# Optimization experiments

Hardware: AMD Instinct MI355X
Metric: run time of the kernel (lower is better)

The kernel has to match this reference:

```python
import jax, jax.numpy as jnp
import numpy as np

D_MODEL = 1024
HEAD_SIZE = 64

def setup_inputs() -> dict:
    key = jax.random.key(0)
    ks = jax.random.split(key, 7)
    s = 1.0 / np.sqrt(D_MODEL)
    return {
        "x": jax.random.normal(ks[0], (4, 2048, D_MODEL), dtype=jnp.float32),
        "wq": jax.random.uniform(ks[1], (D_MODEL, HEAD_SIZE), jnp.float32, -s, s),
        "bq": jax.random.uniform(ks[2], (HEAD_SIZE,), jnp.float32, -s, s),
        "wk": jax.random.uniform(ks[3], (D_MODEL, HEAD_SIZE), jnp.float32, -s, s),
        "bk": jax.random.uniform(ks[4], (HEAD_SIZE,), jnp.float32, -s, s),
        "wv": jax.random.uniform(ks[5], (D_MODEL, HEAD_SIZE), jnp.float32, -s, s),
        "bv": jax.random.uniform(ks[6], (HEAD_SIZE,), jnp.float32, -s, s),
    }

def reference(x, wq, bq, wk, bk, wv, bv):
    # x: [b, n, d_model]; projections -> [b, n, head_size]
    q = x @ wq + bq
    k = x @ wk + bk
    v = x @ wv + bv
    scores = jnp.einsum("bnd,bmd->bnm", q, k) / jnp.sqrt(jnp.float32(HEAD_SIZE))
    attn = jax.nn.softmax(scores, axis=-1)  # [b, n, n]
    return jnp.einsum("bnm,bmd->bnd", attn, v)
```

## Files before the change

kernel.cpp:

```cpp
#include <hip/hip_runtime.h>
#include <math.h>

#define D_MODEL 1024
#define HEAD 64
#define SEQ 2048
#define BATCH 4

typedef _Float16 f16x4 __attribute__((ext_vector_type(4)));
typedef _Float16 f16x8 __attribute__((ext_vector_type(8)));
typedef float f32x4 __attribute__((ext_vector_type(4)));

__global__ __launch_bounds__(256) void prep_w(
    const float* __restrict__ wq, const float* __restrict__ wk,
    const float* __restrict__ wv, _Float16* __restrict__ wT)
{
    const float* w = (blockIdx.y == 0) ? wq : (blockIdx.y == 1) ? wk : wv;
    const int kbase = blockIdx.x * 64;
    __shared__ float t[64][65];
    const int tid = threadIdx.x;
    #pragma unroll
    for (int i = 0; i < 16; i++) {
        int idx = tid + i * 256;
        int kk = idx >> 6, c = idx & 63;
        t[kk][c] = w[(size_t)(kbase + kk) * 64 + c];
    }
    __syncthreads();
    #pragma unroll
    for (int i = 0; i < 16; i++) {
        int idx = tid + i * 256;
        int c = idx >> 6, kk = idx & 63;
        wT[(size_t)(blockIdx.y * 64 + c) * 1024 + kbase + kk] = (_Float16)t[kk][c];
    }
}

__global__ __launch_bounds__(768, 6) void proj_kernel(
    const float* __restrict__ x, const _Float16* __restrict__ wT,
    const float* __restrict__ bq, const float* __restrict__ bk2,
    const float* __restrict__ bv,
    _Float16* __restrict__ q, _Float16* __restrict__ k, _Float16* __restrict__ vT)
{
    const int tid = threadIdx.x;
    const int wave = tid >> 6;
    const int lane = tid & 63;
    const int l16 = lane & 15;
    const int quad = lane >> 4;
    const int row0 = blockIdx.x * 16;

    __shared__ __align__(16) _Float16 Xs[2][16][136];

    const int srow = tid >> 5;
    const int sc4 = tid & 31;
    const float4* xg = reinterpret_cast<const float4*>(x)
                     + (size_t)(row0 + srow) * (D_MODEL / 4) + sc4;

    const _Float16* wp = wT + (size_t)(wave * 16 + l16) * D_MODEL + quad * 8;

    float4 xr;
    if (tid < 512) {
        xr = xg[0];
        f16x4 h;
        h[0] = (_Float16)xr.x; h[1] = (_Float16)xr.y;
        h[2] = (_Float16)xr.z; h[3] = (_Float16)xr.w;
        *(f16x4*)&Xs[0][srow][sc4 * 4] = h;
    }

    f32x4 acc = (f32x4){0.f, 0.f, 0.f, 0.f};

    #pragma unroll 1
    for (int c = 0; c < 8; c++) {
        __syncthreads();
        f16x8 bw0 = *(const f16x8*)(wp + c * 128);
        f16x8 bw1 = *(const f16x8*)(wp + c * 128 + 32);
        f16x8 bw2 = *(const f16x8*)(wp + c * 128 + 64);
        f16x8 bw3 = *(const f16x8*)(wp + c * 128 + 96);
        if (c < 7 && tid < 512) xr = xg[(c + 1) * 32];
        const int bsel = c & 1;
        f16x8 aX0 = *(const f16x8*)&Xs[bsel][l16][0 * 32 + quad * 8];
        f16x8 aX1 = *(const f16x8*)&Xs[bsel][l16][1 * 32 + quad * 8];
        f16x8 aX2 = *(const f16x8*)&Xs[bsel][l16][2 * 32 + quad * 8];
        f16x8 aX3 = *(const f16x8*)&Xs[bsel][l16][3 * 32 + quad * 8];
        acc = __builtin_amdgcn_mfma_f32_16x16x32_f16(aX0, bw0, acc, 0, 0, 0);
        acc = __builtin_amdgcn_mfma_f32_16x16x32_f16(aX1, bw1, acc, 0, 0, 0);
        acc = __builtin_amdgcn_mfma_f32_16x16x32_f16(aX2, bw2, acc, 0, 0, 0);
        acc = __builtin_amdgcn_mfma_f32_16x16x32_f16(aX3, bw3, acc, 0, 0, 0);
        if (c < 7 && tid < 512) {
            f16x4 h;
            h[0] = (_Float16)xr.x; h[1] = (_Float16)xr.y;
            h[2] = (_Float16)xr.z; h[3] = (_Float16)xr.w;
            *(f16x4*)&Xs[bsel ^ 1][srow][sc4 * 4] = h;
        }
    }

    const int g = wave * 16 + l16;
    const int batch = row0 / SEQ;
    const int rbase = row0 + quad * 4;
    if (g < 64) {
        float bias = bq[g];
        #pragma unroll
        for (int r = 0; r < 4; r++)
            q[(size_t)(rbase + r) * HEAD + g] = (_Float16)((acc[r] + bias) * 0.125f);
    } else if (g < 128) {
        float bias = bk2[g - 64];
        #pragma unroll
        for (int r = 0; r < 4; r++)
            k[(size_t)(rbase + r) * HEAD + (g - 64)] = (_Float16)(acc[r] + bias);
    } else {
        float bias = bv[g - 128];
        f16x4 pk;
        #pragma unroll
        for (int r = 0; r < 4; r++) pk[r] = (_Float16)(acc[r] + bias);
        const int seq0 = row0 - batch * SEQ + quad * 4;
        *(f16x4*)(vT + (size_t)(batch * HEAD + (g - 128)) * SEQ + seq0) = pk;
    }
}

__global__ __launch_bounds__(512, 4) void attn_kernel(
    const _Float16* __restrict__ q, const _Float16* __restrict__ k,
    const _Float16* __restrict__ vT, float* __restrict__ out)
{
    const int tid = threadIdx.x;
    const int wave = tid >> 6;
    const int lane = tid & 63;
    const int l16 = lane & 15;
    const int quad = lane >> 4;
    const int b = blockIdx.y;
    const int q0 = blockIdx.x * 16;

    __shared__ __align__(16) char SM[2 * 18432 + 2 * 17408];
    _Float16 (*Ks)[128][72] = (_Float16(*)[128][72])SM;
    _Float16 (*Vs)[64][136] = (_Float16(*)[64][136])(SM + 2 * 18432);
    float (*Oall)[16][68] = (float(*)[16][68])SM;
    __shared__ float Lall[8][16];

    f16x8 bQ[2];
    {
        const _Float16* qp = q + (size_t)(b * SEQ + q0 + l16) * HEAD + quad * 8;
        bQ[0] = *(const f16x8*)qp;
        bQ[1] = *(const f16x8*)(qp + 32);
    }

    f32x4 O[4];
    #pragma unroll
    for (int dt = 0; dt < 4; dt++) O[dt] = (f32x4){0.f, 0.f, 0.f, 0.f};
    float lpart = 0.f;

    const _Float16* kb = k + (size_t)b * SEQ * HEAD;
    const _Float16* vb = vT + (size_t)b * HEAD * SEQ;

    const int krow = tid >> 3, kc8 = (tid & 7) * 8;
    const int vrow = tid >> 4, vc8 = (tid & 15) * 8;
    const _Float16* kg = kb + (size_t)krow * HEAD + kc8;
    const _Float16* vg = vb + (size_t)vrow * SEQ + vc8;

    f16x8 kr0 = *(const f16x8*)kg;
    f16x8 kr1 = *(const f16x8*)(kg + (size_t)64 * HEAD);
    f16x8 vr0 = *(const f16x8*)vg;
    f16x8 vr1 = *(const f16x8*)(vg + (size_t)32 * SEQ);
    *(f16x8*)&Ks[0][krow][kc8] = kr0;
    *(f16x8*)&Ks[0][krow + 64][kc8] = kr1;
    *(f16x8*)&Vs[0][vrow][vc8] = vr0;
    *(f16x8*)&Vs[0][vrow + 32][vc8] = vr1;

    #pragma unroll 1
    for (int c = 0; c < 16; c++) {
        __syncthreads();
        if (c < 15) {
            const int kc2 = (c + 1) * 128;
            kr0 = *(const f16x8*)(kg + (size_t)kc2 * HEAD);
            kr1 = *(const f16x8*)(kg + (size_t)(kc2 + 64) * HEAD);
            vr0 = *(const f16x8*)(vg + kc2);
            vr1 = *(const f16x8*)(vg + (size_t)32 * SEQ + kc2);
        }
        const int bsel = c & 1;
        f16x8 aK0 = *(const f16x8*)&Ks[bsel][wave * 16 + l16][quad * 8];
        f16x8 aK1 = *(const f16x8*)&Ks[bsel][wave * 16 + l16][32 + quad * 8];
        f32x4 st = __builtin_amdgcn_mfma_f32_16x16x32_f16(aK0, bQ[0], (f32x4){0.f, 0.f, 0.f, 0.f}, 0, 0, 0);
        st = __builtin_amdgcn_mfma_f32_16x16x32_f16(aK1, bQ[1], st, 0, 0, 0);

        float p0 = __expf(st[0]);
        float p1 = __expf(st[1]);
        float p2 = __expf(st[2]);
        float p3 = __expf(st[3]);
        lpart += (p0 + p1) + (p2 + p3);
        f16x4 bP;
        bP[0] = (_Float16)p0; bP[1] = (_Float16)p1;
        bP[2] = (_Float16)p2; bP[3] = (_Float16)p3;

        #pragma unroll
        for (int dt = 0; dt < 4; dt++) {
            f16x4 aV = *(const f16x4*)&Vs[bsel][dt * 16 + l16][wave * 16 + quad * 4];
            O[dt] = __builtin_amdgcn_mfma_f32_16x16x16f16(aV, bP, O[dt], 0, 0, 0);
        }
        if (c < 15) {
            *(f16x8*)&Ks[bsel ^ 1][krow][kc8] = kr0;
            *(f16x8*)&Ks[bsel ^ 1][krow + 64][kc8] = kr1;
            *(f16x8*)&Vs[bsel ^ 1][vrow][vc8] = vr0;
            *(f16x8*)&Vs[bsel ^ 1][vrow + 32][vc8] = vr1;
        }
    }
    __syncthreads();

    lpart += __shfl_xor(lpart, 16);
    lpart += __shfl_xor(lpart, 32);
    if (lane < 16) Lall[wave][l16] = lpart;
    #pragma unroll
    for (int dt = 0; dt < 4; dt++)
        #pragma unroll
        for (int r = 0; r < 4; r++)
            Oall[wave][l16][dt * 16 + quad * 4 + r] = O[dt][r];
    __syncthreads();

    {
        int qi = tid >> 5;
        int dd = (tid & 31) * 2;
        float L = 0.f, o0 = 0.f, o1 = 0.f;
        #pragma unroll
        for (int w = 0; w < 8; w++) {
            L += Lall[w][qi];
            o0 += Oall[w][qi][dd];
            o1 += Oall[w][qi][dd + 1];
        }
        float inv = 1.f / L;
        float2 res = make_float2(o0 * inv, o1 * inv);
        *(float2*)(out + (size_t)(b * SEQ + q0 + qi) * HEAD + dd) = res;
    }
}

extern "C" void kernel_launch(void* const* d_in, const int* in_sizes, int n_in,
                              void* d_out, int out_size, void* d_ws, size_t ws_size,
                              hipStream_t stream) {
    const float* x  = (const float*)d_in[0];
    const float* wq = (const float*)d_in[1];
    const float* bq = (const float*)d_in[2];
    const float* wk = (const float*)d_in[3];
    const float* bk = (const float*)d_in[4];
    const float* wv = (const float*)d_in[5];
    const float* bv = (const float*)d_in[6];
    float* out = (float*)d_out;

    const size_t proj_elems = (size_t)BATCH * SEQ * HEAD;
    _Float16* qh = (_Float16*)d_ws;
    _Float16* kh = qh + proj_elems;
    _Float16* vT = kh + proj_elems;
    _Float16* wT = vT + proj_elems;

    prep_w<<<dim3(16, 3), 256, 0, stream>>>(wq, wk, wv, wT);
    proj_kernel<<<dim3(BATCH * SEQ / 16), 768, 0, stream>>>(x, wT, bq, bk, bv, qh, kh, vT);
    attn_kernel<<<dim3(SEQ / 16, BATCH), 512, 0, stream>>>(qh, kh, vT, out);
}
```

Measured before the change: 124.0 us.

## Load K/V fragments directly into registers, process 32 queries per block

The attention kernel no longer stages K and V tiles in shared memory. Each wave loads its own K and transposed-V MFMA fragments straight from global memory into registers, with next-chunk prefetch and no per-iteration barriers. Each block now handles two 16-query tiles so every fragment load feeds twice as much MFMA work, at the cost of more registers and half as many blocks. The projection kernel is fully unrolled and prefetches x four chunks ahead to hide global-load latency.

```diff
diff --git a/kernel.cpp b/kernel.cpp
--- a/kernel.cpp
+++ b/kernel.cpp
@@ -55,25 +55,37 @@
 
     const _Float16* wp = wT + (size_t)(wave * 16 + l16) * D_MODEL + quad * 8;
 
-    float4 xr;
+    float4 xr[4];
     if (tid < 512) {
-        xr = xg[0];
+        xr[0] = xg[0];
+        xr[1] = xg[32];
+        xr[2] = xg[64];
+        xr[3] = xg[96];
         f16x4 h;
-        h[0] = (_Float16)xr.x; h[1] = (_Float16)xr.y;
-        h[2] = (_Float16)xr.z; h[3] = (_Float16)xr.w;
+        h[0] = (_Float16)xr[0].x; h[1] = (_Float16)xr[0].y;
+        h[2] = (_Float16)xr[0].z; h[3] = (_Float16)xr[0].w;
         *(f16x4*)&Xs[0][srow][sc4 * 4] = h;
     }
 
     f32x4 acc = (f32x4){0.f, 0.f, 0.f, 0.f};
 
-    #pragma unroll 1
+    #pragma unroll
     for (int c = 0; c < 8; c++) {
         __syncthreads();
         f16x8 bw0 = *(const f16x8*)(wp + c * 128);
         f16x8 bw1 = *(const f16x8*)(wp + c * 128 + 32);
         f16x8 bw2 = *(const f16x8*)(wp + c * 128 + 64);
         f16x8 bw3 = *(const f16x8*)(wp + c * 128 + 96);
-        if (c < 7 && tid < 512) xr = xg[(c + 1) * 32];
+        if (tid < 512) {
+            if (c + 4 < 8) xr[c & 3] = xg[(c + 4) * 32];
+            if (c < 7) {
+                float4 f = xr[(c + 1) & 3];
+                f16x4 h;
+                h[0] = (_Float16)f.x; h[1] = (_Float16)f.y;
+                h[2] = (_Float16)f.z; h[3] = (_Float16)f.w;
+                *(f16x4*)&Xs[(c + 1) & 1][srow][sc4 * 4] = h;
+            }
+        }
         const int bsel = c & 1;
         f16x8 aX0 = *(const f16x8*)&Xs[bsel][l16][0 * 32 + quad * 8];
         f16x8 aX1 = *(const f16x8*)&Xs[bsel][l16][1 * 32 + quad * 8];
@@ -83,12 +95,6 @@
         acc = __builtin_amdgcn_mfma_f32_16x16x32_f16(aX1, bw1, acc, 0, 0, 0);
         acc = __builtin_amdgcn_mfma_f32_16x16x32_f16(aX2, bw2, acc, 0, 0, 0);
         acc = __builtin_amdgcn_mfma_f32_16x16x32_f16(aX3, bw3, acc, 0, 0, 0);
-        if (c < 7 && tid < 512) {
-            f16x4 h;
-            h[0] = (_Float16)xr.x; h[1] = (_Float16)xr.y;
-            h[2] = (_Float16)xr.z; h[3] = (_Float16)xr.w;
-            *(f16x4*)&Xs[bsel ^ 1][srow][sc4 * 4] = h;
-        }
     }
 
     const int g = wave * 16 + l16;
@@ -124,105 +130,112 @@
     const int l16 = lane & 15;
     const int quad = lane >> 4;
     const int b = blockIdx.y;
-    const int q0 = blockIdx.x * 16;
-
-    __shared__ __align__(16) char SM[2 * 18432 + 2 * 17408];
-    _Float16 (*Ks)[128][72] = (_Float16(*)[128][72])SM;
-    _Float16 (*Vs)[64][136] = (_Float16(*)[64][136])(SM + 2 * 18432);
-    float (*Oall)[16][68] = (float(*)[16][68])SM;
-    __shared__ float Lall[8][16];
-
-    f16x8 bQ[2];
-    {
-        const _Float16* qp = q + (size_t)(b * SEQ + q0 + l16) * HEAD + quad * 8;
-        bQ[0] = *(const f16x8*)qp;
-        bQ[1] = *(const f16x8*)(qp + 32);
-    }
-
-    f32x4 O[4];
-    #pragma unroll
-    for (int dt = 0; dt < 4; dt++) O[dt] = (f32x4){0.f, 0.f, 0.f, 0.f};
-    float lpart = 0.f;
-
-    const _Float16* kb = k + (size_t)b * SEQ * HEAD;
-    const _Float16* vb = vT + (size_t)b * HEAD * SEQ;
-
-    const int krow = tid >> 3, kc8 = (tid & 7) * 8;
-    const int vrow = tid >> 4, vc8 = (tid & 15) * 8;
-    const _Float16* kg = kb + (size_t)krow * HEAD + kc8;
-    const _Float16* vg = vb + (size_t)vrow * SEQ + vc8;
-
-    f16x8 kr0 = *(const f16x8*)kg;
-    f16x8 kr1 = *(const f16x8*)(kg + (size_t)64 * HEAD);
-    f16x8 vr0 = *(const f16x8*)vg;
-    f16x8 vr1 = *(const f16x8*)(vg + (size_t)32 * SEQ);
-    *(f16x8*)&Ks[0][krow][kc8] = kr0;
-    *(f16x8*)&Ks[0][krow + 64][kc8] = kr1;
-    *(f16x8*)&Vs[0][vrow][vc8] = vr0;
-    *(f16x8*)&Vs[0][vrow + 32][vc8] = vr1;
+    const int q0 = blockIdx.x * 32;
+
+    __shared__ float Oall[8][32][68];
+    __shared__ float Lall[8][32];
+
+    f16x8 bQ[2][2];
+    #pragma unroll
+    for (int qt = 0; qt < 2; qt++) {
+        const _Float16* qp = q + (size_t)(b * SEQ + q0 + qt * 16 + l16) * HEAD + quad * 8;
+        bQ[qt][0] = *(const f16x8*)qp;
+        bQ[qt][1] = *(const f16x8*)(qp + 32);
+    }
+
+    f32x4 O[2][4];
+    #pragma unroll
+    for (int qt = 0; qt < 2; qt++)
+        #pragma unroll
+        for (int dt = 0; dt < 4; dt++) O[qt][dt] = (f32x4){0.f, 0.f, 0.f, 0.f};
+    float lp0 = 0.f, lp1 = 0.f;
+
+    const _Float16* kg = k + (size_t)b * SEQ * HEAD
+                       + (size_t)(wave * 16 + l16) * HEAD + quad * 8;
+    const _Float16* vg = vT + (size_t)b * HEAD * SEQ
+                       + (size_t)l16 * SEQ + wave * 16 + quad * 4;
+
+    f16x8 ck0 = *(const f16x8*)kg;
+    f16x8 ck1 = *(const f16x8*)(kg + 32);
+    f16x4 cv0 = *(const f16x4*)(vg);
+    f16x4 cv1 = *(const f16x4*)(vg + 16 * SEQ);
+    f16x4 cv2 = *(const f16x4*)(vg + 32 * SEQ);
+    f16x4 cv3 = *(const f16x4*)(vg + 48 * SEQ);
 
     #pragma unroll 1
     for (int c = 0; c < 16; c++) {
-        __syncthreads();
+        f16x8 nk0, nk1;
+        f16x4 nv0, nv1, nv2, nv3;
         if (c < 15) {
-            const int kc2 = (c + 1) * 128;
-            kr0 = *(const f16x8*)(kg + (size_t)kc2 * HEAD);
-            kr1 = *(const f16x8*)(kg + (size_t)(kc2 + 64) * HEAD);
-            vr0 = *(const f16x8*)(vg + kc2);
-            vr1 = *(const f16x8*)(vg + (size_t)32 * SEQ + kc2);
-        }
-        const int bsel = c & 1;
-        f16x8 aK0 = *(const f16x8*)&Ks[bsel][wave * 16 + l16][quad * 8];
-        f16x8 aK1 = *(const f16x8*)&Ks[bsel][wave * 16 + l16][32 + quad * 8];
-        f32x4 st = __builtin_amdgcn_mfma_f32_16x16x32_f16(aK0, bQ[0], (f32x4){0.f, 0.f, 0.f, 0.f}, 0, 0, 0);
-        st = __builtin_amdgcn_mfma_f32_16x16x32_f16(aK1, bQ[1], st, 0, 0, 0);
-
-        float p0 = __expf(st[0]);
-        float p1 = __expf(st[1]);
-        float p2 = __expf(st[2]);
-        float p3 = __expf(st[3]);
-        lpart += (p0 + p1) + (p2 + p3);
-        f16x4 bP;
-        bP[0] = (_Float16)p0; bP[1] = (_Float16)p1;
-        bP[2] = (_Float16)p2; bP[3] = (_Float16)p3;
-
-        #pragma unroll
-        for (int dt = 0; dt < 4; dt++) {
-            f16x4 aV = *(const f16x4*)&Vs[bsel][dt * 16 + l16][wave * 16 + quad * 4];
-            O[dt] = __builtin_amdgcn_mfma_f32_16x16x16f16(aV, bP, O[dt], 0, 0, 0);
+            const _Float16* kp = kg + (size_t)(c + 1) * 128 * HEAD;
+            nk0 = *(const f16x8*)kp;
+            nk1 = *(const f16x8*)(kp + 32);
+            const _Float16* vp = vg + (c + 1) * 128;
+            nv0 = *(const f16x4*)(vp);
+            nv1 = *(const f16x4*)(vp + 16 * SEQ);
+            nv2 = *(const f16x4*)(vp + 32 * SEQ);
+            nv3 = *(const f16x4*)(vp + 48 * SEQ);
+        }
+        f16x4 bP[2];
+        #pragma unroll
+        for (int qt = 0; qt < 2; qt++) {
+            f32x4 st = __builtin_amdgcn_mfma_f32_16x16x32_f16(ck0, bQ[qt][0], (f32x4){0.f, 0.f, 0.f, 0.f}, 0, 0, 0);
+            st = __builtin_amdgcn_mfma_f32_16x16x32_f16(ck1, bQ[qt][1], st, 0, 0, 0);
+            float p0 = __expf(st[0]);
+            float p1 = __expf(st[1]);
+            float p2 = __expf(st[2]);
+            float p3 = __expf(st[3]);
+            if (qt == 0) lp0 += (p0 + p1) + (p2 + p3);
+            else         lp1 += (p0 + p1) + (p2 + p3);
+            f16x4 bp;
+            bp[0] = (_Float16)p0; bp[1] = (_Float16)p1;
+            bp[2] = (_Float16)p2; bp[3] = (_Float16)p3;
+            bP[qt] = bp;
+        }
+        #pragma unroll
+        for (int qt = 0; qt < 2; qt++) {
+            O[qt][0] = __builtin_amdgcn_mfma_f32_16x16x16f16(cv0, bP[qt], O[qt][0], 0, 0, 0);
+            O[qt][1] = __builtin_amdgcn_mfma_f32_16x16x16f16(cv1, bP[qt], O[qt][1], 0, 0, 0);
+            O[qt][2] = __builtin_amdgcn_mfma_f32_16x16x16f16(cv2, bP[qt], O[qt][2], 0, 0, 0);
+            O[qt][3] = __builtin_amdgcn_mfma_f32_16x16x16f16(cv3, bP[qt], O[qt][3], 0, 0, 0);
         }
         if (c < 15) {
-            *(f16x8*)&Ks[bsel ^ 1][krow][kc8] = kr0;
-            *(f16x8*)&Ks[bsel ^ 1][krow + 64][kc8] = kr1;
-            *(f16x8*)&Vs[bsel ^ 1][vrow][vc8] = vr0;
-            *(f16x8*)&Vs[bsel ^ 1][vrow + 32][vc8] = vr1;
-        }
-    }
+            ck0 = nk0; ck1 = nk1;
+            cv0 = nv0; cv1 = nv1; cv2 = nv2; cv3 = nv3;
+        }
+    }
+
+    lp0 += __shfl_xor(lp0, 16); lp0 += __shfl_xor(lp0, 32);
+    lp1 += __shfl_xor(lp1, 16); lp1 += __shfl_xor(lp1, 32);
+    if (lane < 16) {
+        Lall[wave][l16] = lp0;
+        Lall[wave][16 + l16] = lp1;
+    }
+    #pragma unroll
+    for (int qt = 0; qt < 2; qt++)
+        #pragma unroll
+        for (int dt = 0; dt < 4; dt++)
+            #pragma unroll
+            for (int r = 0; r < 4; r++)
+                Oall[wave][qt * 16 + l16][dt * 16 + quad * 4 + r] = O[qt][dt][r];
     __syncthreads();
 
-    lpart += __shfl_xor(lpart, 16);
-    lpart += __shfl_xor(lpart, 32);
-    if (lane < 16) Lall[wave][l16] = lpart;
-    #pragma unroll
-    for (int dt = 0; dt < 4; dt++)
-        #pragma unroll
-        for (int r = 0; r < 4; r++)
-            Oall[wave][l16][dt * 16 + quad * 4 + r] = O[dt][r];
-    __syncthreads();
-
     {
-        int qi = tid >> 5;
-        int dd = (tid & 31) * 2;
-        float L = 0.f, o0 = 0.f, o1 = 0.f;
+        int qi = tid >> 4;
+        int dg = tid & 15;
+        float L = 0.f;
+        float o[4] = {0.f, 0.f, 0.f, 0.f};
         #pragma unroll
         for (int w = 0; w < 8; w++) {
             L += Lall[w][qi];
-            o0 += Oall[w][qi][dd];
-            o1 += Oall[w][qi][dd + 1];
+            #pragma unroll
+            for (int j = 0; j < 4; j++) o[j] += Oall[w][qi][dg * 4 + j];
         }
         float inv = 1.f / L;
-        float2 res = make_float2(o0 * inv, o1 * inv);
-        *(float2*)(out + (size_t)(b * SEQ + q0 + qi) * HEAD + dd) = res;
+        float4 res;
+        res.x = o[0] * inv; res.y = o[1] * inv;
+        res.z = o[2] * inv; res.w = o[3] * inv;
+        *(float4*)(out + (size_t)(b * SEQ + q0 + qi) * HEAD + dg * 4) = res;
     }
 }
 
@@ -246,5 +259,5 @@
 
     prep_w<<<dim3(16, 3), 256, 0, stream>>>(wq, wk, wv, wT);
     proj_kernel<<<dim3(BATCH * SEQ / 16), 768, 0, stream>>>(x, wT, bq, bk, bv, qh, kh, vT);
-    attn_kernel<<<dim3(SEQ / 16, BATCH), 512, 0, stream>>>(qh, kh, vT, out);
-}
+    attn_kernel<<<dim3(SEQ / 32, BATCH), 512, 0, stream>>>(qh, kh, vT, out);
+}
```

Measured after the change: 131.0 us. 5.7% more time.

## Split projection kernel into dedicated producer wave loading x and MFMA consumer waves

Applied to the files above, without the earlier changes.

Adds a 13th wave (896 threads) to the projection kernel that only loads fp32 x rows, converts them to fp16 and writes the double-buffered LDS tile. The 12 compute waves now only load weights and issue MFMAs. Previously the first 8 compute waves also carried the x loads. The intent is warp specialization, so global x loads overlap with MFMA work. The cost is a larger block and a lower occupancy target (7 waves per SIMD-limited bound). The producer still waits at the same per-chunk barrier, so load latency is only hidden by one stage of prefetch.

```diff
diff --git a/kernel.cpp b/kernel.cpp
--- a/kernel.cpp
+++ b/kernel.cpp
@@ -33,7 +33,7 @@
     }
 }
 
-__global__ __launch_bounds__(768, 6) void proj_kernel(
+__global__ __launch_bounds__(896, 7) void proj_kernel(
     const float* __restrict__ x, const _Float16* __restrict__ wT,
     const float* __restrict__ bq, const float* __restrict__ bk2,
     const float* __restrict__ bv,
@@ -48,20 +48,31 @@
 
     __shared__ __align__(16) _Float16 Xs[2][16][136];
 
-    const int srow = tid >> 5;
-    const int sc4 = tid & 31;
-    const float4* xg = reinterpret_cast<const float4*>(x)
-                     + (size_t)(row0 + srow) * (D_MODEL / 4) + sc4;
+    const bool producer = (wave >= 12);
+
+    const int tid2 = tid - 768;
+    const int srow = (tid2 >> 3) & 15;
+    const int kg = (tid2 & 7) * 16;
+    const float* xp = x + (size_t)(row0 + srow) * D_MODEL + kg;
 
     const _Float16* wp = wT + (size_t)(wave * 16 + l16) * D_MODEL + quad * 8;
 
-    float4 xr;
-    if (tid < 512) {
-        xr = xg[0];
-        f16x4 h;
-        h[0] = (_Float16)xr.x; h[1] = (_Float16)xr.y;
-        h[2] = (_Float16)xr.z; h[3] = (_Float16)xr.w;
-        *(f16x4*)&Xs[0][srow][sc4 * 4] = h;
+    if (producer) {
+        float4 f0 = *(const float4*)(xp);
+        float4 f1 = *(const float4*)(xp + 4);
+        float4 f2 = *(const float4*)(xp + 8);
+        float4 f3 = *(const float4*)(xp + 12);
+        f16x8 h0, h1;
+        h0[0] = (_Float16)f0.x; h0[1] = (_Float16)f0.y;
+        h0[2] = (_Float16)f0.z; h0[3] = (_Float16)f0.w;
+        h0[4] = (_Float16)f1.x; h0[5] = (_Float16)f1.y;
+        h0[6] = (_Float16)f1.z; h0[7] = (_Float16)f1.w;
+        h1[0] = (_Float16)f2.x; h1[1] = (_Float16)f2.y;
+        h1[2] = (_Float16)f2.z; h1[3] = (_Float16)f2.w;
+        h1[4] = (_Float16)f3.x; h1[5] = (_Float16)f3.y;
+        h1[6] = (_Float16)f3.z; h1[7] = (_Float16)f3.w;
+        *(f16x8*)&Xs[0][srow][kg] = h0;
+        *(f16x8*)&Xs[0][srow][kg + 8] = h1;
     }
 
     f32x4 acc = (f32x4){0.f, 0.f, 0.f, 0.f};
@@ -69,48 +80,63 @@
     #pragma unroll 1
     for (int c = 0; c < 8; c++) {
         __syncthreads();
-        f16x8 bw0 = *(const f16x8*)(wp + c * 128);
-        f16x8 bw1 = *(const f16x8*)(wp + c * 128 + 32);
-        f16x8 bw2 = *(const f16x8*)(wp + c * 128 + 64);
-        f16x8 bw3 = *(const f16x8*)(wp + c * 128 + 96);
-        if (c < 7 && tid < 512) xr = xg[(c + 1) * 32];
-        const int bsel = c & 1;
-        f16x8 aX0 = *(const f16x8*)&Xs[bsel][l16][0 * 32 + quad * 8];
-        f16x8 aX1 = *(const f16x8*)&Xs[bsel][l16][1 * 32 + quad * 8];
-        f16x8 aX2 = *(const f16x8*)&Xs[bsel][l16][2 * 32 + quad * 8];
-        f16x8 aX3 = *(const f16x8*)&Xs[bsel][l16][3 * 32 + quad * 8];
-        acc = __builtin_amdgcn_mfma_f32_16x16x32_f16(aX0, bw0, acc, 0, 0, 0);
-        acc = __builtin_amdgcn_mfma_f32_16x16x32_f16(aX1, bw1, acc, 0, 0, 0);
-        acc = __builtin_amdgcn_mfma_f32_16x16x32_f16(aX2, bw2, acc, 0, 0, 0);
-        acc = __builtin_amdgcn_mfma_f32_16x16x32_f16(aX3, bw3, acc, 0, 0, 0);
-        if (c < 7 && tid < 512) {
-            f16x4 h;
-            h[0] = (_Float16)xr.x; h[1] = (_Float16)xr.y;
-            h[2] = (_Float16)xr.z; h[3] = (_Float16)xr.w;
-            *(f16x4*)&Xs[bsel ^ 1][srow][sc4 * 4] = h;
-        }
-    }
-
-    const int g = wave * 16 + l16;
-    const int batch = row0 / SEQ;
-    const int rbase = row0 + quad * 4;
-    if (g < 64) {
-        float bias = bq[g];
-        #pragma unroll
-        for (int r = 0; r < 4; r++)
-            q[(size_t)(rbase + r) * HEAD + g] = (_Float16)((acc[r] + bias) * 0.125f);
-    } else if (g < 128) {
-        float bias = bk2[g - 64];
-        #pragma unroll
-        for (int r = 0; r < 4; r++)
-            k[(size_t)(rbase + r) * HEAD + (g - 64)] = (_Float16)(acc[r] + bias);
-    } else {
-        float bias = bv[g - 128];
-        f16x4 pk;
-        #pragma unroll
-        for (int r = 0; r < 4; r++) pk[r] = (_Float16)(acc[r] + bias);
-        const int seq0 = row0 - batch * SEQ + quad * 4;
-        *(f16x4*)(vT + (size_t)(batch * HEAD + (g - 128)) * SEQ + seq0) = pk;
+        if (!producer) {
+            f16x8 bw0 = *(const f16x8*)(wp + c * 128);
+            f16x8 bw1 = *(const f16x8*)(wp + c * 128 + 32);
+            f16x8 bw2 = *(const f16x8*)(wp + c * 128 + 64);
+            f16x8 bw3 = *(const f16x8*)(wp + c * 128 + 96);
+            const int bsel = c & 1;
+            f16x8 aX0 = *(const f16x8*)&Xs[bsel][l16][0 * 32 + quad * 8];
+            f16x8 aX1 = *(const f16x8*)&Xs[bsel][l16][1 * 32 + quad * 8];
+            f16x8 aX2 = *(const f16x8*)&Xs[bsel][l16][2 * 32 + quad * 8];
+            f16x8 aX3 = *(const f16x8*)&Xs[bsel][l16][3 * 32 + quad * 8];
+            acc = __builtin_amdgcn_mfma_f32_16x16x32_f16(aX0, bw0, acc, 0, 0, 0);
+            acc = __builtin_amdgcn_mfma_f32_16x16x32_f16(aX1, bw1, acc, 0, 0, 0);
+            acc = __builtin_amdgcn_mfma_f32_16x16x32_f16(aX2, bw2, acc, 0, 0, 0);
+            acc = __builtin_amdgcn_mfma_f32_16x16x32_f16(aX3, bw3, acc, 0, 0, 0);
+        } else if (c < 7) {
+            const float* p = xp + (c + 1) * 128;
+            float4 f0 = *(const float4*)(p);
+            float4 f1 = *(const float4*)(p + 4);
+            float4 f2 = *(const float4*)(p + 8);
+            float4 f3 = *(const float4*)(p + 12);
+            f16x8 h0, h1;
+            h0[0] = (_Float16)f0.x; h0[1] = (_Float16)f0.y;
+            h0[2] = (_Float16)f0.z; h0[3] = (_Float16)f0.w;
+            h0[4] = (_Float16)f1.x; h0[5] = (_Float16)f1.y;
+            h0[6] = (_Float16)f1.z; h0[7] = (_Float16)f1.w;
+            h1[0] = (_Float16)f2.x; h1[1] = (_Float16)f2.y;
+            h1[2] = (_Float16)f2.z; h1[3] = (_Float16)f2.w;
+            h1[4] = (_Float16)f3.x; h1[5] = (_Float16)f3.y;
+            h1[6] = (_Float16)f3.z; h1[7] = (_Float16)f3.w;
+            const int nb = (c + 1) & 1;
+            *(f16x8*)&Xs[nb][srow][kg] = h0;
+            *(f16x8*)&Xs[nb][srow][kg + 8] = h1;
+        }
+    }
+
+    if (!producer) {
+        const int g = wave * 16 + l16;
+        const int batch = row0 / SEQ;
+        const int rbase = row0 + quad * 4;
+        if (g < 64) {
+            float bias = bq[g];
+            #pragma unroll
+            for (int r = 0; r < 4; r++)
+                q[(size_t)(rbase + r) * HEAD + g] = (_Float16)((acc[r] + bias) * 0.125f);
+        } else if (g < 128) {
+            float bias = bk2[g - 64];
+            #pragma unroll
+            for (int r = 0; r < 4; r++)
+                k[(size_t)(rbase + r) * HEAD + (g - 64)] = (_Float16)(acc[r] + bias);
+        } else {
+            float bias = bv[g - 128];
+            f16x4 pk;
+            #pragma unroll
+            for (int r = 0; r < 4; r++) pk[r] = (_Float16)(acc[r] + bias);
+            const int seq0 = row0 - batch * SEQ + quad * 4;
+            *(f16x4*)(vT + (size_t)(batch * HEAD + (g - 128)) * SEQ + seq0) = pk;
+        }
     }
 }
 
@@ -245,6 +271,6 @@
     _Float16* wT = vT + proj_elems;
 
     prep_w<<<dim3(16, 3), 256, 0, stream>>>(wq, wk, wv, wT);
-    proj_kernel<<<dim3(BATCH * SEQ / 16), 768, 0, stream>>>(x, wT, bq, bk, bv, qh, kh, vT);
+    proj_kernel<<<dim3(BATCH * SEQ / 16), 896, 0, stream>>>(x, wT, bq, bk, bv, qh, kh, vT);
     attn_kernel<<<dim3(SEQ / 16, BATCH), 512, 0, stream>>>(qh, kh, vT, out);
 }
```

Result: slower. 127.5 us (+2.9%).
